# Kernel tuning notes

Hardware: AMD Instinct MI355X
Metric: run time of the kernel (lower is better)

## Reference

```python
import jax, jax.numpy as jnp
import numpy as np

B, L, C = 2, 8192, 256
K, NLEV = 17, 4
HALF = K // 2


def setup_inputs() -> dict:
    key = jax.random.key(0)
    ks = jax.random.split(key, 10)
    s = 0.02
    return {
        "x": jax.random.normal(ks[0], (B, L, C), jnp.float32),
        "stem_w": jax.random.normal(ks[1], (C, C, 2), jnp.float32) * s,   # Conv1d (out,in,k)
        "stem_b": jax.random.normal(ks[2], (C,), jnp.float32) * s,
        "qkv_w": jax.random.normal(ks[3], (3 * C, C), jnp.float32) * s,
        "width_w": jax.random.normal(ks[4], (1, C), jnp.float32) * s,
        "width_b": jax.random.normal(ks[5], (1,), jnp.float32) * s,
        "out_w": jax.random.normal(ks[6], (C, C), jnp.float32) * s,
        "query": jax.random.normal(ks[7], (NLEV * C,), jnp.float32) * s,
        "film_w": jax.random.normal(ks[8], (2 * C, NLEV * C), jnp.float32) * s,
        "film_b": jax.random.normal(ks[9], (2 * C,), jnp.float32) * s,
    }


def _local_attn(h, qkv_w, width_w, width_b, out_w):
    # h: (b, l, c); 1D local windowed attention with learned sigmoid distance mask
    b, l, c = h.shape
    rel_dist = jnp.abs(jnp.arange(K, dtype=h.dtype) - HALF)  # (K,)
    max_dist = float(HALF)
    scale = c ** -0.5
    qkv = h @ qkv_w.T
    q, k, v = jnp.split(qkv, 3, axis=-1)
    width = jax.nn.sigmoid(h @ width_w.T + width_b) * max_dist + 0.5  # (b,l,1)
    k_pad = jnp.pad(k, ((0, 0), (HALF, HALF), (0, 0)))
    v_pad = jnp.pad(v, ((0, 0), (HALF, HALF), (0, 0)))
    idx = jnp.arange(l)[:, None] + jnp.arange(K)[None, :]  # (l,K) indices into padded seq
    k_win = k_pad[:, idx]  # (b,l,K,c)
    v_win = v_pad[:, idx]  # (b,l,K,c)
    scores = jnp.einsum('blc,blwc->blw', q, k_win) * scale
    soft_mask = jax.nn.sigmoid((width - rel_dist) * 5.0)  # (b,l,K)
    scores = scores - (1.0 - soft_mask) * 10000.0
    attn = jax.nn.softmax(scores, axis=-1)
    o = jnp.einsum('blw,blwc->blc', attn, v_win)
    return (o + v) @ out_w.T


def _forward(x, stem_w, stem_b, qkv_w, width_w, width_b, out_w, query, film_w, film_b):
    b, l, c = x.shape
    # stem conv: Conv1d(C, C, kernel=2, padding=1), then narrow to first l positions
    h = jnp.transpose(x, (0, 2, 1))  # (B,C,L)
    h = jax.lax.conv_general_dilated(h, stem_w, (1,), [(1, 1)],
                                     dimension_numbers=('NCH', 'OIH', 'NCH'))
    h = h[:, :, :l] + stem_b[None, :, None]
    h = jnp.transpose(h, (0, 2, 1))  # (B,L,C)
    levels = []
    for i in range(NLEV):
        h = _local_attn(h, qkv_w, width_w, width_b, out_w)
        levels.append(h)
        if i < NLEV - 1:  # avg_pool(kernel=2, stride=2)
            bl = h.shape[1]
            h = h.reshape(b, bl // 2, 2, c).mean(axis=2)
    # nearest upsample each coarser level back to L (factors are exact powers of 2)
    ups = [levels[0]]
    for lvl in levels[1:]:
        ups.append(jnp.repeat(lvl, l // lvl.shape[1], axis=1))
    concat = jnp.concatenate(ups, axis=-1)  # (B,L,NLEV*C)
    gattn = jax.nn.softmax(concat @ query, axis=-1)  # (B,L)
    global_ctx = jnp.einsum('bl,bld->bd', gattn, concat)  # (B,NLEV*C)
    film = global_ctx @ film_w.T + film_b  # (B,2C)
    scale_f, bias_f = jnp.split(film, 2, axis=-1)
    return levels[0] * (1.0 + scale_f[:, None, :]) + bias_f[:, None, :]


def reference(x, stem_w, stem_b, qkv_w, width_w, width_b, out_w, query, film_w, film_b):
    return _forward(x, stem_w, stem_b, qkv_w, width_w, width_b, out_w, query, film_w, film_b)
```

## Files before the change

kernel.cpp:

```cpp
#include <hip/hip_runtime.h>
#include <math.h>

#define L_SEQ 8192
#define B_SZ  2
#define CH    256
#define NLEV  4

typedef __attribute__((ext_vector_type(8))) short bf16x8;
typedef __attribute__((ext_vector_type(4))) float f32x4;

static __device__ __forceinline__ float sigmoidf_(float x) {
    return 1.0f / (1.0f + expf(-x));
}

static __device__ __forceinline__ float bf2f_(unsigned short u) {
    union { unsigned int ui; float f; } x;
    x.ui = ((unsigned int)u) << 16;
    return x.f;
}
static __device__ __forceinline__ unsigned short f2b_(float f) {
    union { float f; unsigned int u; } x;
    x.f = f;
    unsigned int lsb = (x.u >> 16) & 1u;
    unsigned int r = x.u + 0x7fffu + lsb;
    return (unsigned short)(r >> 16);
}
static __device__ __forceinline__ float4 ldb4_(const unsigned short* p) {
    ushort4 u = *(const ushort4*)p;
    return make_float4(bf2f_(u.x), bf2f_(u.y), bf2f_(u.z), bf2f_(u.w));
}

#define NPREP_BLOCKS 17409
__global__ __launch_bounds__(256) void prep_kernel(
    const float* __restrict__ x, const float* __restrict__ qkv_w,
    const float* __restrict__ out_w, const float* __restrict__ stem_w,
    unsigned short* __restrict__ x16g, unsigned short* __restrict__ qw16,
    unsigned short* __restrict__ sw16)
{
    __shared__ float owr[256];
    if (blockIdx.x >= NPREP_BLOCKS) {
        const int c = blockIdx.x - NPREP_BLOCKS, j = threadIdx.x;
        owr[j] = out_w[(size_t)c * 256 + j];
        __syncthreads();
        float acc = 0.0f;
        #pragma unroll 8
        for (int k = 0; k < 256; ++k)
            acc += owr[k] * qkv_w[(size_t)(512 + k) * 256 + j];
        qw16[(size_t)(512 + c) * 256 + j] = f2b_(acc);
        return;
    }
    int i = blockIdx.x * 256 + threadIdx.x;
    if (i < 256) { x16g[i] = 0; return; }
    i -= 256;
    if (i < 4194304) { x16g[256 + i] = f2b_(x[i]); return; }
    i -= 4194304;
    if (i < 131072) { qw16[i] = f2b_(qkv_w[i]); return; }
    i -= 131072;
    {
        int k = i & 511, nn = i >> 9;
        float v = (k < 256) ? stem_w[(size_t)nn * 512 + k * 2]
                            : stem_w[(size_t)nn * 512 + (k - 256) * 2 + 1];
        sw16[i] = f2b_(v);
    }
}

template<int STEM>
__global__ __launch_bounds__(512, 2) void level_fused_kernel(
    const unsigned short* __restrict__ h16in, const unsigned short* __restrict__ x16g,
    const unsigned short* __restrict__ sw, const float* __restrict__ sbias,
    const unsigned short* __restrict__ qw,
    const float* __restrict__ ww, const float* __restrict__ wbp,
    unsigned short* __restrict__ l16o, unsigned short* __restrict__ dsB, int l)
{
    __shared__ __align__(16) char smem[127232];
    unsigned short* hs = (unsigned short*)smem;
    unsigned short* xs = (unsigned short*)(smem + 40960);
    unsigned short* qs = (unsigned short*)(smem + 40960);
    unsigned short* ks = (unsigned short*)(smem + 73728);
    unsigned short* vt = (unsigned short*)(smem + 40960);
    unsigned short* pb = (unsigned short*)(smem + 114688);
    float* sp1 = (float*)(smem + 118784);
    float* ws1 = (float*)(smem + 126976);

    const int tid  = threadIdx.x;
    const int wave = tid >> 6;
    const int lane = tid & 63;
    const int rt   = wave & 3;
    const int half = wave >> 2;
    const int q    = lane >> 4;
    const int n    = lane & 15;

    int bid = blockIdx.x;
    const int cpx = gridDim.x >> 3;
    bid = (bid & 7) * cpx + (bid >> 3);

    const int bps = l >> 6;
    const int b  = bid / bps;
    const int t0 = (bid % bps) << 6;
    const size_t seqbase = (size_t)b * l;
    const int row0 = t0 + rt * 16;
    const int ct0 = wave * 2;

    if constexpr (STEM) {
        #pragma unroll
        for (int i = 0; i < 6; ++i) {
            const int task = i * 512 + tid;
            if (task < 2592) {
                const int r = task >> 5, ch = task & 31;
                const int gx = t0 - 9 + r;
                const unsigned short* src = (gx >= 0 && gx < l)
                    ? x16g + ((size_t)(seqbase + gx) + 1) * 256 + ((ch ^ (r & 7)) << 3)
                    : x16g;
                __builtin_amdgcn_global_load_lds(
                    (const __attribute__((address_space(1))) void*)src,
                    (__attribute__((address_space(3))) void*)
                        (xs + (size_t)(i * 512 + (tid & ~63)) * 8),
                    16, 0, 0);
            }
        }
        __syncthreads();

        f32x4 accA[5] = {}, accB[5] = {};
        #pragma unroll
        for (int pass = 0; pass < 2; ++pass) {
            bf16x8 wA[8], wB[8];
            const unsigned short* wa_ = sw + (size_t)(ct0 * 16 + n) * 512 + pass * 256 + q * 8;
            const unsigned short* wb_ = sw + (size_t)((ct0 + 1) * 16 + n) * 512 + pass * 256 + q * 8;
            #pragma unroll
            for (int j = 0; j < 8; ++j) {
                wA[j] = *(const bf16x8*)(wa_ + j * 32);
                wB[j] = *(const bf16x8*)(wb_ + j * 32);
            }
            #pragma unroll
            for (int rtile = 0; rtile < 5; ++rtile) {
                const int xr = rtile * 16 + n + pass;
                const int xswz = (xr & 7) << 4;
                bf16x8 af[8];
                #pragma unroll
                for (int j = 0; j < 8; ++j)
                    af[j] = *(const bf16x8*)((const char*)xs +
                             ((xr * 512 + (j * 32 + q * 8) * 2) ^ xswz));
                #pragma unroll
                for (int j = 0; j < 8; ++j) {
                    accA[rtile] = __builtin_amdgcn_mfma_f32_16x16x32_bf16(af[j], wA[j], accA[rtile], 0, 0, 0);
                    accB[rtile] = __builtin_amdgcn_mfma_f32_16x16x32_bf16(af[j], wB[j], accB[rtile], 0, 0, 0);
                }
            }
        }
        const float bA = sbias[ct0 * 16 + n];
        const float bB = sbias[(ct0 + 1) * 16 + n];
        #pragma unroll
        for (int rtile = 0; rtile < 5; ++rtile)
            #pragma unroll
            for (int idx = 0; idx < 4; ++idx) {
                const int row = rtile * 16 + q * 4 + idx;
                const int growh = t0 - 8 + row;
                const int rswz = (row & 7) << 4;
                const bool ok = (growh >= 0 && growh < l);
                *(unsigned short*)((char*)hs +
                    ((row * 512 + (ct0 * 16 + n) * 2) ^ rswz)) =
                        ok ? f2b_(accA[rtile][idx] + bA) : (unsigned short)0;
                *(unsigned short*)((char*)hs +
                    ((row * 512 + ((ct0 + 1) * 16 + n) * 2) ^ rswz)) =
                        ok ? f2b_(accB[rtile][idx] + bB) : (unsigned short)0;
            }
        __syncthreads();
    } else {
        #pragma unroll
        for (int i = 0; i < 5; ++i) {
            const int task = i * 512 + tid;
            const int r = task >> 5, ch = task & 31;
            const int grow = t0 - 8 + r;
            const unsigned short* src = (grow >= 0 && grow < l)
                ? h16in + (seqbase + grow) * 256 + ((ch ^ (r & 7)) << 3)
                : x16g;
            __builtin_amdgcn_global_load_lds(
                (const __attribute__((address_space(1))) void*)src,
                (__attribute__((address_space(3))) void*)
                    (hs + (size_t)(i * 512 + (tid & ~63)) * 8),
                16, 0, 0);
        }
        __syncthreads();
    }

    {
        bf16x8 bwa[8], bwb[8];
        const unsigned short* wa_ = qw + (size_t)(ct0 * 16 + n) * 256 + q * 8;
        const unsigned short* wb_ = qw + (size_t)((ct0 + 1) * 16 + n) * 256 + q * 8;
        #pragma unroll
        for (int j = 0; j < 8; ++j) {
            bwa[j] = *(const bf16x8*)(wa_ + j * 32);
            bwb[j] = *(const bf16x8*)(wb_ + j * 32);
        }
        #pragma unroll
        for (int rtq = 0; rtq < 4; ++rtq) {
            const int hr = 8 + rtq * 16 + n;
            const int hswz = (hr & 7) << 4;
            bf16x8 af[8];
            #pragma unroll
            for (int j = 0; j < 8; ++j)
                af[j] = *(const bf16x8*)((const char*)hs +
                         ((hr * 512 + (j * 32 + q * 8) * 2) ^ hswz));
            f32x4 aA = {}, aB = {};
            #pragma unroll
            for (int j = 0; j < 8; ++j) {
                aA = __builtin_amdgcn_mfma_f32_16x16x32_bf16(af[j], bwa[j], aA, 0, 0, 0);
                aB = __builtin_amdgcn_mfma_f32_16x16x32_bf16(af[j], bwb[j], aB, 0, 0, 0);
            }
            #pragma unroll
            for (int idx = 0; idx < 4; ++idx) {
                const int row = rtq * 16 + q * 4 + idx;
                const int rswz = (row & 7) << 4;
                *(unsigned short*)((char*)qs +
                    ((row * 512 + (ct0 * 16 + n) * 2) ^ rswz)) = f2b_(aA[idx]);
                *(unsigned short*)((char*)qs +
                    ((row * 512 + ((ct0 + 1) * 16 + n) * 2) ^ rswz)) = f2b_(aB[idx]);
            }
        }
    }
    {
        bf16x8 bwa[8], bwb[8];
        const unsigned short* wa_ = qw + (size_t)(256 + ct0 * 16 + n) * 256 + q * 8;
        const unsigned short* wb_ = qw + (size_t)(256 + (ct0 + 1) * 16 + n) * 256 + q * 8;
        #pragma unroll
        for (int j = 0; j < 8; ++j) {
            bwa[j] = *(const bf16x8*)(wa_ + j * 32);
            bwb[j] = *(const bf16x8*)(wb_ + j * 32);
        }
        #pragma unroll
        for (int rtk = 0; rtk < 5; ++rtk) {
            const int hr = rtk * 16 + n;
            const int hswz = (hr & 7) << 4;
            bf16x8 af[8];
            #pragma unroll
            for (int j = 0; j < 8; ++j)
                af[j] = *(const bf16x8*)((const char*)hs +
                         ((hr * 512 + (j * 32 + q * 8) * 2) ^ hswz));
            f32x4 aA = {}, aB = {};
            #pragma unroll
            for (int j = 0; j < 8; ++j) {
                aA = __builtin_amdgcn_mfma_f32_16x16x32_bf16(af[j], bwa[j], aA, 0, 0, 0);
                aB = __builtin_amdgcn_mfma_f32_16x16x32_bf16(af[j], bwb[j], aB, 0, 0, 0);
            }
            #pragma unroll
            for (int idx = 0; idx < 4; ++idx) {
                const int row = rtk * 16 + q * 4 + idx;
                const int rswz = (row & 7) << 4;
                *(unsigned short*)((char*)ks +
                    ((row * 512 + (ct0 * 16 + n) * 2) ^ rswz)) = f2b_(aA[idx]);
                *(unsigned short*)((char*)ks +
                    ((row * 512 + ((ct0 + 1) * 16 + n) * 2) ^ rswz)) = f2b_(aB[idx]);
            }
        }
    }
    __syncthreads();

    const int kc0 = half * 128;
    float wdot = 0.0f;
    {
        const int hr = 8 + rt * 16 + n;
        const int hswz = (hr & 7) << 4;
        #pragma unroll
        for (int jj = 0; jj < 4; ++jj) {
            bf16x8 hv = *(const bf16x8*)((const char*)hs +
                        ((hr * 512 + (kc0 + q * 32 + jj * 8) * 2) ^ hswz));
            float4 wa = *((const float4*)(ww + kc0 + q * 32 + jj * 8));
            float4 wc = *((const float4*)(ww + kc0 + q * 32 + jj * 8 + 4));
            wdot += bf2f_((unsigned short)hv[0]) * wa.x
                  + bf2f_((unsigned short)hv[1]) * wa.y
                  + bf2f_((unsigned short)hv[2]) * wa.z
                  + bf2f_((unsigned short)hv[3]) * wa.w
                  + bf2f_((unsigned short)hv[4]) * wc.x
                  + bf2f_((unsigned short)hv[5]) * wc.y
                  + bf2f_((unsigned short)hv[6]) * wc.z
                  + bf2f_((unsigned short)hv[7]) * wc.w;
        }
    }
    wdot += __shfl_xor(wdot, 16, 64);
    wdot += __shfl_xor(wdot, 32, 64);
    if (half == 1 && q == 0) ws1[rt * 16 + n] = wdot;

    f32x4 accS[2] = {};
    {
        const int qrow = rt * 16 + n;
        const int qswz = (qrow & 7) << 4;
        bf16x8 qf[4];
        #pragma unroll
        for (int j = 0; j < 4; ++j)
            qf[j] = *(const bf16x8*)((const char*)qs +
                     ((qrow * 512 + (kc0 + q * 8 + j * 32) * 2) ^ qswz));
        #pragma unroll
        for (int h = 0; h < 2; ++h) {
            const int rk = rt * 16 + h * 16 + n;
            const int kswz = (rk & 7) << 4;
            #pragma unroll
            for (int j = 0; j < 4; ++j) {
                bf16x8 kb = *(const bf16x8*)((const char*)ks +
                            ((rk * 512 + (kc0 + q * 8 + j * 32) * 2) ^ kswz));
                accS[h] = __builtin_amdgcn_mfma_f32_16x16x32_bf16(
                    qf[j], kb, accS[h], 0, 0, 0);
            }
        }
    }
    if (half == 1) {
        *(f32x4*)(sp1 + ((rt * 2 + 0) * 64 + lane) * 4) = accS[0];
        *(f32x4*)(sp1 + ((rt * 2 + 1) * 64 + lane) * 4) = accS[1];
    }
    __syncthreads();

    if (half == 0) {
        accS[0] += *(const f32x4*)(sp1 + ((rt * 2 + 0) * 64 + lane) * 4);
        accS[1] += *(const f32x4*)(sp1 + ((rt * 2 + 1) * 64 + lane) * 4);
        const float w_n = sigmoidf_(wdot + ws1[rt * 16 + n] + wbp[0]) * 8.0f + 0.5f;

        float wd[4];
        #pragma unroll
        for (int r = 0; r < 4; ++r) wd[r] = __shfl(w_n, q * 4 + r, 64);

        float s[2][4];
        #pragma unroll
        for (int h = 0; h < 2; ++h)
            #pragma unroll
            for (int r = 0; r < 4; ++r) {
                int ii = q * 4 + r;
                int c  = h * 16 + n;
                int w  = c - ii;
                float dist = fabsf((float)w - 8.0f);
                float sm = sigmoidf_((wd[r] - dist) * 5.0f);
                float v = accS[h][r] * 0.0625f - (1.0f - sm) * 10000.0f;
                s[h][r] = (w >= 0 && w <= 16) ? v : -3.0e38f;
            }

        float mx[4], sum[4];
        #pragma unroll
        for (int r = 0; r < 4; ++r) mx[r] = fmaxf(s[0][r], s[1][r]);
        #pragma unroll
        for (int m = 1; m < 16; m <<= 1)
            #pragma unroll
            for (int r = 0; r < 4; ++r) mx[r] = fmaxf(mx[r], __shfl_xor(mx[r], m, 64));
        float e[2][4];
        #pragma unroll
        for (int h = 0; h < 2; ++h)
            #pragma unroll
            for (int r = 0; r < 4; ++r) e[h][r] = expf(s[h][r] - mx[r]);
        #pragma unroll
        for (int r = 0; r < 4; ++r) sum[r] = e[0][r] + e[1][r];
        #pragma unroll
        for (int m = 1; m < 16; m <<= 1)
            #pragma unroll
            for (int r = 0; r < 4; ++r) sum[r] += __shfl_xor(sum[r], m, 64);

        #pragma unroll
        for (int h = 0; h < 2; ++h)
            #pragma unroll
            for (int r = 0; r < 4; ++r) {
                int ii = q * 4 + r, c = h * 16 + n;
                float p = e[h][r] / sum[r];
                if (c == ii + 8) p += 1.0f;
                pb[rt * 512 + ii * 32 + c] = f2b_(p);
            }
    }
    __syncthreads();

    {
        bf16x8 bwa[8], bwb[8];
        const unsigned short* wa_ = qw + (size_t)(512 + ct0 * 16 + n) * 256 + q * 8;
        const unsigned short* wb_ = qw + (size_t)(512 + (ct0 + 1) * 16 + n) * 256 + q * 8;
        #pragma unroll
        for (int j = 0; j < 8; ++j) {
            bwa[j] = *(const bf16x8*)(wa_ + j * 32);
            bwb[j] = *(const bf16x8*)(wb_ + j * 32);
        }
        #pragma unroll
        for (int rtv = 0; rtv < 5; ++rtv) {
            const int hr = rtv * 16 + n;
            const int hswz = (hr & 7) << 4;
            bf16x8 af[8];
            #pragma unroll
            for (int j = 0; j < 8; ++j)
                af[j] = *(const bf16x8*)((const char*)hs +
                         ((hr * 512 + (j * 32 + q * 8) * 2) ^ hswz));
            f32x4 aA = {}, aB = {};
            #pragma unroll
            for (int j = 0; j < 8; ++j) {
                aA = __builtin_amdgcn_mfma_f32_16x16x32_bf16(af[j], bwa[j], aA, 0, 0, 0);
                aB = __builtin_amdgcn_mfma_f32_16x16x32_bf16(af[j], bwb[j], aB, 0, 0, 0);
            }
            ushort4 pA, pB;
            pA.x = f2b_(aA[0]); pA.y = f2b_(aA[1]); pA.z = f2b_(aA[2]); pA.w = f2b_(aA[3]);
            pB.x = f2b_(aB[0]); pB.y = f2b_(aB[1]); pB.z = f2b_(aB[2]); pB.w = f2b_(aB[3]);
            const int rb = rtv * 16 + q * 4;
            *(ushort4*)(vt + (size_t)(ct0 * 16 + n) * 88 + rb) = pA;
            *(ushort4*)(vt + (size_t)((ct0 + 1) * 16 + n) * 88 + rb) = pB;
        }
    }
    __syncthreads();

    bf16x8 pf = *(const bf16x8*)(pb + rt * 512 + n * 32 + q * 8);
    const int rl = q * 4;
    const size_t gbase = seqbase + row0;
    #pragma unroll
    for (int c = 0; c < 8; ++c) {
        const int ct = half * 8 + c;
        bf16x8 vf = *(const bf16x8*)(vt + (ct * 16 + n) * 88 + rt * 16 + q * 8);
        f32x4 z = {};
        f32x4 o = __builtin_amdgcn_mfma_f32_16x16x32_bf16(pf, vf, z, 0, 0, 0);
        const int col = ct * 16 + n;
        float v0 = o[0], v1 = o[1], v2 = o[2], v3 = o[3];
        size_t r0 = (gbase + rl) * CH + col;
        l16o[r0]          = f2b_(v0);
        l16o[r0 + CH]     = f2b_(v1);
        l16o[r0 + 2 * CH] = f2b_(v2);
        l16o[r0 + 3 * CH] = f2b_(v3);
        if (dsB) {
            size_t d0 = ((gbase + rl) >> 1) * CH + col;
            dsB[d0]      = f2b_(0.5f * (v0 + v1));
            dsB[d0 + CH] = f2b_(0.5f * (v2 + v3));
        }
    }
}

__global__ __launch_bounds__(1024) void tail_ctx_kernel(
    const unsigned short* __restrict__ l0, const unsigned short* __restrict__ l1,
    const unsigned short* __restrict__ l2, const unsigned short* __restrict__ l3,
    const float* __restrict__ query, float* __restrict__ partials,
    float* __restrict__ denomP)
{
    __shared__ float eS[128];
    const int tid = threadIdx.x;
    const int chunk = blockIdx.x, b = blockIdx.y;
    const int t0 = chunk * 128;
    const unsigned short* levp[4] = {l0, l1, l2, l3};

    const int w = tid >> 6, lane = tid & 63;
    const int lev = lane >> 4, c0 = (lane & 15) * 16;
    const unsigned short* lpbase = levp[lev] + (size_t)b * (L_SEQ >> lev) * CH;
    const float* qp = query + lev * CH + c0;
    float4 q0 = *(const float4*)(qp);
    float4 q1 = *(const float4*)(qp + 4);
    float4 q2 = *(const float4*)(qp + 8);
    float4 q3 = *(const float4*)(qp + 12);
    #pragma unroll
    for (int j = 0; j < 8; ++j) {
        int t = t0 + w * 8 + j;
        const unsigned short* p = lpbase + (size_t)(t >> lev) * CH + c0;
        float4 h0 = ldb4_(p), h1 = ldb4_(p + 4), h2 = ldb4_(p + 8), h3 = ldb4_(p + 12);
        float part = h0.x * q0.x + h0.y * q0.y + h0.z * q0.z + h0.w * q0.w
                   + h1.x * q1.x + h1.y * q1.y + h1.z * q1.z + h1.w * q1.w
                   + h2.x * q2.x + h2.y * q2.y + h2.z * q2.z + h2.w * q2.w
                   + h3.x * q3.x + h3.y * q3.y + h3.z * q3.z + h3.w * q3.w;
        #pragma unroll
        for (int m = 1; m < 64; m <<= 1) part += __shfl_xor(part, m, 64);
        if (lane == 0) eS[w * 8 + j] = expf(part);
    }
    __syncthreads();

    if (tid == 0) {
        float ds = 0.0f;
        #pragma unroll 8
        for (int i = 0; i < 128; ++i) ds += eS[i];
        denomP[b * 64 + chunk] = ds;
    }

    const int dlev = tid >> 8, c = tid & 255;
    const unsigned short* lp = levp[dlev] + (size_t)b * (L_SEQ >> dlev) * CH;
    float acc = 0.0f;
    #pragma unroll 4
    for (int t = t0; t < t0 + 128; ++t)
        acc += eS[t - t0] * bf2f_(lp[(size_t)(t >> dlev) * CH + c]);
    partials[(size_t)(b * 64 + chunk) * 1024 + tid] = acc;
}

__global__ __launch_bounds__(256) void film_kernel(
    const float* __restrict__ partials, const float* __restrict__ denomP,
    const float* __restrict__ fw, const float* __restrict__ fb,
    float* __restrict__ film)
{
    __shared__ float ctxS[2048];
    const int tid = threadIdx.x;

    float den[2];
    #pragma unroll
    for (int b = 0; b < 2; ++b) {
        float d = 0.0f;
        #pragma unroll
        for (int c = 0; c < 64; ++c) d += denomP[b * 64 + c];
        den[b] = d;
    }
    #pragma unroll
    for (int v = 0; v < 8; ++v) {
        const int idx = v * 256 + tid;
        const int b = idx >> 10, d = idx & 1023;
        float acc = 0.0f;
        #pragma unroll
        for (int c = 0; c < 64; ++c)
            acc += partials[(size_t)(b * 64 + c) * 1024 + d];
        ctxS[idx] = acc / den[b];
    }
    __syncthreads();

    const int lane = tid & 63;
    const int j = blockIdx.x * 4 + (tid >> 6);
    float acc0 = 0.0f, acc1 = 0.0f;
    #pragma unroll
    for (int r = 0; r < 4; ++r) {
        float4 w4 = *((const float4*)(fw + (size_t)j * 1024 + r * 256) + lane);
        float4 c0 = *((const float4*)(ctxS + r * 256) + lane);
        float4 c1 = *((const float4*)(ctxS + 1024 + r * 256) + lane);
        acc0 += w4.x * c0.x + w4.y * c0.y + w4.z * c0.z + w4.w * c0.w;
        acc1 += w4.x * c1.x + w4.y * c1.y + w4.z * c1.z + w4.w * c1.w;
    }
    #pragma unroll
    for (int m = 1; m < 64; m <<= 1) {
        acc0 += __shfl_xor(acc0, m, 64);
        acc1 += __shfl_xor(acc1, m, 64);
    }
    if (lane == 0) {
        float b = fb[j];
        film[j] = acc0 + b;
        film[512 + j] = acc1 + b;
    }
}

__global__ void final_kernel(const unsigned short* __restrict__ lev0,
                             const float* __restrict__ film,
                             float* __restrict__ out)
{
    size_t n4 = ((size_t)blockIdx.x * 256 + threadIdx.x) * 4;
    int c = (int)(n4 & (CH - 1));
    int b = (int)(n4 >> 21);
    float4 h = ldb4_(lev0 + n4);
    const float* fs = film + b * 512;
    float4 o;
    o.x = h.x * (1.0f + fs[c + 0]) + fs[256 + c + 0];
    o.y = h.y * (1.0f + fs[c + 1]) + fs[256 + c + 1];
    o.z = h.z * (1.0f + fs[c + 2]) + fs[256 + c + 2];
    o.w = h.w * (1.0f + fs[c + 3]) + fs[256 + c + 3];
    *(float4*)(out + n4) = o;
}

extern "C" void kernel_launch(void* const* d_in, const int* in_sizes, int n_in,
                              void* d_out, int out_size, void* d_ws, size_t ws_size,
                              hipStream_t stream) {
    const float* x       = (const float*)d_in[0];
    const float* stem_w  = (const float*)d_in[1];
    const float* stem_b  = (const float*)d_in[2];
    const float* qkv_w   = (const float*)d_in[3];
    const float* width_w = (const float*)d_in[4];
    const float* width_b = (const float*)d_in[5];
    const float* out_w   = (const float*)d_in[6];
    const float* query   = (const float*)d_in[7];
    const float* film_w  = (const float*)d_in[8];
    const float* film_b  = (const float*)d_in[9];
    float* out = (float*)d_out;
    float* ws  = (float*)d_ws;

    float* partials = ws;
    float* denomP   = partials + 131072;
    float* ctx      = denomP + 128;
    float* film     = ctx + 2048;
    unsigned short* x16g  = (unsigned short*)(film + 1024);
    unsigned short* h16_0 = x16g + 4194560;
    unsigned short* h16_1 = h16_0 + 4194304;
    unsigned short* h16_2 = h16_1 + 2097152;
    unsigned short* h16_3 = h16_2 + 1048576;
    unsigned short* qkv16 = h16_3 + 524288;
    unsigned short* ov16  = qkv16 + 12582912;
    unsigned short* l16_0 = ov16 + 4194304;
    unsigned short* l16_1 = l16_0 + 4194304;
    unsigned short* l16_2 = l16_1 + 2097152;
    unsigned short* l16_3 = l16_2 + 1048576;
    unsigned short* qw16  = l16_3 + 524288;
    unsigned short* ow16  = qw16 + 196608;
    unsigned short* sw16  = ow16 + 65536;
    unsigned short* h16[4]  = {h16_0, h16_1, h16_2, h16_3};
    unsigned short* l16[4]  = {l16_0, l16_1, l16_2, l16_3};
    (void)qkv16; (void)ov16; (void)ow16; (void)ctx;

    prep_kernel<<<NPREP_BLOCKS + 256, 256, 0, stream>>>(
        x, qkv_w, out_w, stem_w, x16g, qw16, sw16);

    for (int i = 0; i < NLEV; ++i) {
        const int l = L_SEQ >> i;
        const int M = B_SZ * l;
        if (i == 0)
            level_fused_kernel<1><<<M / 64, 512, 0, stream>>>(
                h16[0], x16g, sw16, stem_b, qw16, width_w, width_b,
                l16[0], h16_1, l);
        else
            level_fused_kernel<0><<<M / 64, 512, 0, stream>>>(
                h16[i], x16g, sw16, stem_b, qw16, width_w, width_b,
                l16[i], (i < NLEV - 1) ? h16[i + 1] : nullptr, l);
    }

    tail_ctx_kernel<<<dim3(64, B_SZ), 1024, 0, stream>>>(
        l16_0, l16_1, l16_2, l16_3, query, partials, denomP);
    film_kernel<<<128, 256, 0, stream>>>(partials, denomP, film_w, film_b, film);
    final_kernel<<<(B_SZ * L_SEQ * CH) / 1024, 256, 0, stream>>>(l16_0, film, out);
}
```

Before: 225.5 us.

## Double block to 1024 threads with one column tile per wave

The fused level kernel now launches 1024 threads (16 waves) per block instead of 512. Each wave handles one 16-column output tile in the stem, Q, K and V projections instead of two, and the PV output stage is split across all 16 waves. Only 8 waves do the score and width work and 4 do the softmax, so some waves sit idle during those phases. The aim is more waves per block to hide latency and halve per-wave register use. Shared memory of about 127 KB per block already limited residency, so one larger block replaces the two smaller ones per CU.

```diff
diff --git a/kernel.cpp b/kernel.cpp
--- a/kernel.cpp
+++ b/kernel.cpp
@@ -65,7 +65,7 @@
 }
 
 template<int STEM>
-__global__ __launch_bounds__(512, 2) void level_fused_kernel(
+__global__ __launch_bounds__(1024, 1) void level_fused_kernel(
     const unsigned short* __restrict__ h16in, const unsigned short* __restrict__ x16g,
     const unsigned short* __restrict__ sw, const float* __restrict__ sbias,
     const unsigned short* __restrict__ qw,
@@ -85,10 +85,11 @@
     const int tid  = threadIdx.x;
     const int wave = tid >> 6;
     const int lane = tid & 63;
-    const int rt   = wave & 3;
-    const int half = wave >> 2;
+    const int rt8  = wave & 3;
+    const int half = (wave >> 2) & 1;
     const int q    = lane >> 4;
     const int n    = lane & 15;
+    const int ct   = wave;
 
     int bid = blockIdx.x;
     const int cpx = gridDim.x >> 3;
@@ -98,13 +99,11 @@
     const int b  = bid / bps;
     const int t0 = (bid % bps) << 6;
     const size_t seqbase = (size_t)b * l;
-    const int row0 = t0 + rt * 16;
-    const int ct0 = wave * 2;
 
     if constexpr (STEM) {
         #pragma unroll
-        for (int i = 0; i < 6; ++i) {
-            const int task = i * 512 + tid;
+        for (int i = 0; i < 3; ++i) {
+            const int task = i * 1024 + tid;
             if (task < 2592) {
                 const int r = task >> 5, ch = task & 31;
                 const int gx = t0 - 9 + r;
@@ -114,23 +113,19 @@
                 __builtin_amdgcn_global_load_lds(
                     (const __attribute__((address_space(1))) void*)src,
                     (__attribute__((address_space(3))) void*)
-                        (xs + (size_t)(i * 512 + (tid & ~63)) * 8),
+                        (xs + (size_t)(i * 1024 + (tid & ~63)) * 8),
                     16, 0, 0);
             }
         }
         __syncthreads();
 
-        f32x4 accA[5] = {}, accB[5] = {};
+        f32x4 accA[5] = {};
         #pragma unroll
         for (int pass = 0; pass < 2; ++pass) {
-            bf16x8 wA[8], wB[8];
-            const unsigned short* wa_ = sw + (size_t)(ct0 * 16 + n) * 512 + pass * 256 + q * 8;
-            const unsigned short* wb_ = sw + (size_t)((ct0 + 1) * 16 + n) * 512 + pass * 256 + q * 8;
-            #pragma unroll
-            for (int j = 0; j < 8; ++j) {
-                wA[j] = *(const bf16x8*)(wa_ + j * 32);
-                wB[j] = *(const bf16x8*)(wb_ + j * 32);
-            }
+            bf16x8 wA[8];
+            const unsigned short* wa_ = sw + (size_t)(ct * 16 + n) * 512 + pass * 256 + q * 8;
+            #pragma unroll
+            for (int j = 0; j < 8; ++j) wA[j] = *(const bf16x8*)(wa_ + j * 32);
             #pragma unroll
             for (int rtile = 0; rtile < 5; ++rtile) {
                 const int xr = rtile * 16 + n + pass;
@@ -141,14 +136,12 @@
                     af[j] = *(const bf16x8*)((const char*)xs +
                              ((xr * 512 + (j * 32 + q * 8) * 2) ^ xswz));
                 #pragma unroll
-                for (int j = 0; j < 8; ++j) {
-                    accA[rtile] = __builtin_amdgcn_mfma_f32_16x16x32_bf16(af[j], wA[j], accA[rtile], 0, 0, 0);
-                    accB[rtile] = __builtin_amdgcn_mfma_f32_16x16x32_bf16(af[j], wB[j], accB[rtile], 0, 0, 0);
-                }
-            }
-        }
-        const float bA = sbias[ct0 * 16 + n];
-        const float bB = sbias[(ct0 + 1) * 16 + n];
+                for (int j = 0; j < 8; ++j)
+                    accA[rtile] = __builtin_amdgcn_mfma_f32_16x16x32_bf16(
+                        af[j], wA[j], accA[rtile], 0, 0, 0);
+            }
+        }
+        const float bA = sbias[ct * 16 + n];
         #pragma unroll
         for (int rtile = 0; rtile < 5; ++rtile)
             #pragma unroll
@@ -158,40 +151,35 @@
                 const int rswz = (row & 7) << 4;
                 const bool ok = (growh >= 0 && growh < l);
                 *(unsigned short*)((char*)hs +
-                    ((row * 512 + (ct0 * 16 + n) * 2) ^ rswz)) =
+                    ((row * 512 + (ct * 16 + n) * 2) ^ rswz)) =
                         ok ? f2b_(accA[rtile][idx] + bA) : (unsigned short)0;
-                *(unsigned short*)((char*)hs +
-                    ((row * 512 + ((ct0 + 1) * 16 + n) * 2) ^ rswz)) =
-                        ok ? f2b_(accB[rtile][idx] + bB) : (unsigned short)0;
             }
         __syncthreads();
     } else {
         #pragma unroll
-        for (int i = 0; i < 5; ++i) {
-            const int task = i * 512 + tid;
-            const int r = task >> 5, ch = task & 31;
-            const int grow = t0 - 8 + r;
-            const unsigned short* src = (grow >= 0 && grow < l)
-                ? h16in + (seqbase + grow) * 256 + ((ch ^ (r & 7)) << 3)
-                : x16g;
-            __builtin_amdgcn_global_load_lds(
-                (const __attribute__((address_space(1))) void*)src,
-                (__attribute__((address_space(3))) void*)
-                    (hs + (size_t)(i * 512 + (tid & ~63)) * 8),
-                16, 0, 0);
+        for (int i = 0; i < 3; ++i) {
+            const int task = i * 1024 + tid;
+            if (task < 2560) {
+                const int r = task >> 5, ch = task & 31;
+                const int grow = t0 - 8 + r;
+                const unsigned short* src = (grow >= 0 && grow < l)
+                    ? h16in + (seqbase + grow) * 256 + ((ch ^ (r & 7)) << 3)
+                    : x16g;
+                __builtin_amdgcn_global_load_lds(
+                    (const __attribute__((address_space(1))) void*)src,
+                    (__attribute__((address_space(3))) void*)
+                        (hs + (size_t)(i * 1024 + (tid & ~63)) * 8),
+                    16, 0, 0);
+            }
         }
         __syncthreads();
     }
 
     {
-        bf16x8 bwa[8], bwb[8];
-        const unsigned short* wa_ = qw + (size_t)(ct0 * 16 + n) * 256 + q * 8;
-        const unsigned short* wb_ = qw + (size_t)((ct0 + 1) * 16 + n) * 256 + q * 8;
-        #pragma unroll
-        for (int j = 0; j < 8; ++j) {
-            bwa[j] = *(const bf16x8*)(wa_ + j * 32);
-            bwb[j] = *(const bf16x8*)(wb_ + j * 32);
-        }
+        bf16x8 bwa[8];
+        const unsigned short* wa_ = qw + (size_t)(ct * 16 + n) * 256 + q * 8;
+        #pragma unroll
+        for (int j = 0; j < 8; ++j) bwa[j] = *(const bf16x8*)(wa_ + j * 32);
         #pragma unroll
         for (int rtq = 0; rtq < 4; ++rtq) {
             const int hr = 8 + rtq * 16 + n;
@@ -201,32 +189,24 @@
             for (int j = 0; j < 8; ++j)
                 af[j] = *(const bf16x8*)((const char*)hs +
                          ((hr * 512 + (j * 32 + q * 8) * 2) ^ hswz));
-            f32x4 aA = {}, aB = {};
-            #pragma unroll
-            for (int j = 0; j < 8; ++j) {
+            f32x4 aA = {};
+            #pragma unroll
+            for (int j = 0; j < 8; ++j)
                 aA = __builtin_amdgcn_mfma_f32_16x16x32_bf16(af[j], bwa[j], aA, 0, 0, 0);
-                aB = __builtin_amdgcn_mfma_f32_16x16x32_bf16(af[j], bwb[j], aB, 0, 0, 0);
-            }
             #pragma unroll
             for (int idx = 0; idx < 4; ++idx) {
                 const int row = rtq * 16 + q * 4 + idx;
                 const int rswz = (row & 7) << 4;
                 *(unsigned short*)((char*)qs +
-                    ((row * 512 + (ct0 * 16 + n) * 2) ^ rswz)) = f2b_(aA[idx]);
-                *(unsigned short*)((char*)qs +
-                    ((row * 512 + ((ct0 + 1) * 16 + n) * 2) ^ rswz)) = f2b_(aB[idx]);
+                    ((row * 512 + (ct * 16 + n) * 2) ^ rswz)) = f2b_(aA[idx]);
             }
         }
     }
     {
-        bf16x8 bwa[8], bwb[8];
-        const unsigned short* wa_ = qw + (size_t)(256 + ct0 * 16 + n) * 256 + q * 8;
-        const unsigned short* wb_ = qw + (size_t)(256 + (ct0 + 1) * 16 + n) * 256 + q * 8;
-        #pragma unroll
-        for (int j = 0; j < 8; ++j) {
-            bwa[j] = *(const bf16x8*)(wa_ + j * 32);
-            bwb[j] = *(const bf16x8*)(wb_ + j * 32);
-        }
+        bf16x8 bwa[8];
+        const unsigned short* wa_ = qw + (size_t)(256 + ct * 16 + n) * 256 + q * 8;
+        #pragma unroll
+        for (int j = 0; j < 8; ++j) bwa[j] = *(const bf16x8*)(wa_ + j * 32);
         #pragma unroll
         for (int rtk = 0; rtk < 5; ++rtk) {
             const int hr = rtk * 16 + n;
@@ -236,82 +216,80 @@
             for (int j = 0; j < 8; ++j)
                 af[j] = *(const bf16x8*)((const char*)hs +
                          ((hr * 512 + (j * 32 + q * 8) * 2) ^ hswz));
-            f32x4 aA = {}, aB = {};
-            #pragma unroll
-            for (int j = 0; j < 8; ++j) {
+            f32x4 aA = {};
+            #pragma unroll
+            for (int j = 0; j < 8; ++j)
                 aA = __builtin_amdgcn_mfma_f32_16x16x32_bf16(af[j], bwa[j], aA, 0, 0, 0);
-                aB = __builtin_amdgcn_mfma_f32_16x16x32_bf16(af[j], bwb[j], aB, 0, 0, 0);
-            }
             #pragma unroll
             for (int idx = 0; idx < 4; ++idx) {
                 const int row = rtk * 16 + q * 4 + idx;
                 const int rswz = (row & 7) << 4;
                 *(unsigned short*)((char*)ks +
-                    ((row * 512 + (ct0 * 16 + n) * 2) ^ rswz)) = f2b_(aA[idx]);
-                *(unsigned short*)((char*)ks +
-                    ((row * 512 + ((ct0 + 1) * 16 + n) * 2) ^ rswz)) = f2b_(aB[idx]);
+                    ((row * 512 + (ct * 16 + n) * 2) ^ rswz)) = f2b_(aA[idx]);
             }
         }
     }
     __syncthreads();
 
-    const int kc0 = half * 128;
     float wdot = 0.0f;
-    {
-        const int hr = 8 + rt * 16 + n;
-        const int hswz = (hr & 7) << 4;
-        #pragma unroll
-        for (int jj = 0; jj < 4; ++jj) {
-            bf16x8 hv = *(const bf16x8*)((const char*)hs +
-                        ((hr * 512 + (kc0 + q * 32 + jj * 8) * 2) ^ hswz));
-            float4 wa = *((const float4*)(ww + kc0 + q * 32 + jj * 8));
-            float4 wc = *((const float4*)(ww + kc0 + q * 32 + jj * 8 + 4));
-            wdot += bf2f_((unsigned short)hv[0]) * wa.x
-                  + bf2f_((unsigned short)hv[1]) * wa.y
-                  + bf2f_((unsigned short)hv[2]) * wa.z
-                  + bf2f_((unsigned short)hv[3]) * wa.w
-                  + bf2f_((unsigned short)hv[4]) * wc.x
-                  + bf2f_((unsigned short)hv[5]) * wc.y
-                  + bf2f_((unsigned short)hv[6]) * wc.z
-                  + bf2f_((unsigned short)hv[7]) * wc.w;
-        }
-    }
-    wdot += __shfl_xor(wdot, 16, 64);
-    wdot += __shfl_xor(wdot, 32, 64);
-    if (half == 1 && q == 0) ws1[rt * 16 + n] = wdot;
-
     f32x4 accS[2] = {};
-    {
-        const int qrow = rt * 16 + n;
-        const int qswz = (qrow & 7) << 4;
-        bf16x8 qf[4];
-        #pragma unroll
-        for (int j = 0; j < 4; ++j)
-            qf[j] = *(const bf16x8*)((const char*)qs +
-                     ((qrow * 512 + (kc0 + q * 8 + j * 32) * 2) ^ qswz));
-        #pragma unroll
-        for (int h = 0; h < 2; ++h) {
-            const int rk = rt * 16 + h * 16 + n;
-            const int kswz = (rk & 7) << 4;
-            #pragma unroll
-            for (int j = 0; j < 4; ++j) {
-                bf16x8 kb = *(const bf16x8*)((const char*)ks +
-                            ((rk * 512 + (kc0 + q * 8 + j * 32) * 2) ^ kswz));
-                accS[h] = __builtin_amdgcn_mfma_f32_16x16x32_bf16(
-                    qf[j], kb, accS[h], 0, 0, 0);
-            }
-        }
-    }
-    if (half == 1) {
-        *(f32x4*)(sp1 + ((rt * 2 + 0) * 64 + lane) * 4) = accS[0];
-        *(f32x4*)(sp1 + ((rt * 2 + 1) * 64 + lane) * 4) = accS[1];
+    if (wave < 8) {
+        const int kc0 = half * 128;
+        {
+            const int hr = 8 + rt8 * 16 + n;
+            const int hswz = (hr & 7) << 4;
+            #pragma unroll
+            for (int jj = 0; jj < 4; ++jj) {
+                bf16x8 hv = *(const bf16x8*)((const char*)hs +
+                            ((hr * 512 + (kc0 + q * 32 + jj * 8) * 2) ^ hswz));
+                float4 wa = *((const float4*)(ww + kc0 + q * 32 + jj * 8));
+                float4 wc = *((const float4*)(ww + kc0 + q * 32 + jj * 8 + 4));
+                wdot += bf2f_((unsigned short)hv[0]) * wa.x
+                      + bf2f_((unsigned short)hv[1]) * wa.y
+                      + bf2f_((unsigned short)hv[2]) * wa.z
+                      + bf2f_((unsigned short)hv[3]) * wa.w
+                      + bf2f_((unsigned short)hv[4]) * wc.x
+                      + bf2f_((unsigned short)hv[5]) * wc.y
+                      + bf2f_((unsigned short)hv[6]) * wc.z
+                      + bf2f_((unsigned short)hv[7]) * wc.w;
+            }
+        }
+        wdot += __shfl_xor(wdot, 16, 64);
+        wdot += __shfl_xor(wdot, 32, 64);
+        if (half == 1 && q == 0) ws1[rt8 * 16 + n] = wdot;
+
+        {
+            const int qrow = rt8 * 16 + n;
+            const int qswz = (qrow & 7) << 4;
+            bf16x8 qf[4];
+            #pragma unroll
+            for (int j = 0; j < 4; ++j)
+                qf[j] = *(const bf16x8*)((const char*)qs +
+                         ((qrow * 512 + (kc0 + q * 8 + j * 32) * 2) ^ qswz));
+            #pragma unroll
+            for (int h = 0; h < 2; ++h) {
+                const int rk = rt8 * 16 + h * 16 + n;
+                const int kswz = (rk & 7) << 4;
+                #pragma unroll
+                for (int j = 0; j < 4; ++j) {
+                    bf16x8 kb = *(const bf16x8*)((const char*)ks +
+                                ((rk * 512 + (kc0 + q * 8 + j * 32) * 2) ^ kswz));
+                    accS[h] = __builtin_amdgcn_mfma_f32_16x16x32_bf16(
+                        qf[j], kb, accS[h], 0, 0, 0);
+                }
+            }
+        }
+        if (half == 1) {
+            *(f32x4*)(sp1 + ((rt8 * 2 + 0) * 64 + lane) * 4) = accS[0];
+            *(f32x4*)(sp1 + ((rt8 * 2 + 1) * 64 + lane) * 4) = accS[1];
+        }
     }
     __syncthreads();
 
-    if (half == 0) {
-        accS[0] += *(const f32x4*)(sp1 + ((rt * 2 + 0) * 64 + lane) * 4);
-        accS[1] += *(const f32x4*)(sp1 + ((rt * 2 + 1) * 64 + lane) * 4);
-        const float w_n = sigmoidf_(wdot + ws1[rt * 16 + n] + wbp[0]) * 8.0f + 0.5f;
+    if (wave < 4) {
+        accS[0] += *(const f32x4*)(sp1 + ((rt8 * 2 + 0) * 64 + lane) * 4);
+        accS[1] += *(const f32x4*)(sp1 + ((rt8 * 2 + 1) * 64 + lane) * 4);
+        const float w_n = sigmoidf_(wdot + ws1[rt8 * 16 + n] + wbp[0]) * 8.0f + 0.5f;
 
         float wd[4];
         #pragma unroll
@@ -357,20 +335,16 @@
                 int ii = q * 4 + r, c = h * 16 + n;
                 float p = e[h][r] / sum[r];
                 if (c == ii + 8) p += 1.0f;
-                pb[rt * 512 + ii * 32 + c] = f2b_(p);
+                pb[rt8 * 512 + ii * 32 + c] = f2b_(p);
             }
     }
     __syncthreads();
 
     {
-        bf16x8 bwa[8], bwb[8];
-        const unsigned short* wa_ = qw + (size_t)(512 + ct0 * 16 + n) * 256 + q * 8;
-        const unsigned short* wb_ = qw + (size_t)(512 + (ct0 + 1) * 16 + n) * 256 + q * 8;
-        #pragma unroll
-        for (int j = 0; j < 8; ++j) {
-            bwa[j] = *(const bf16x8*)(wa_ + j * 32);
-            bwb[j] = *(const bf16x8*)(wb_ + j * 32);
-        }
+        bf16x8 bwa[8];
+        const unsigned short* wa_ = qw + (size_t)(512 + ct * 16 + n) * 256 + q * 8;
+        #pragma unroll
+        for (int j = 0; j < 8; ++j) bwa[j] = *(const bf16x8*)(wa_ + j * 32);
         #pragma unroll
         for (int rtv = 0; rtv < 5; ++rtv) {
             const int hr = rtv * 16 + n;
@@ -380,42 +354,43 @@
             for (int j = 0; j < 8; ++j)
                 af[j] = *(const bf16x8*)((const char*)hs +
                          ((hr * 512 + (j * 32 + q * 8) * 2) ^ hswz));
-            f32x4 aA = {}, aB = {};
-            #pragma unroll
-            for (int j = 0; j < 8; ++j) {
+            f32x4 aA = {};
+            #pragma unroll
+            for (int j = 0; j < 8; ++j)
                 aA = __builtin_amdgcn_mfma_f32_16x16x32_bf16(af[j], bwa[j], aA, 0, 0, 0);
-                aB = __builtin_amdgcn_mfma_f32_16x16x32_bf16(af[j], bwb[j], aB, 0, 0, 0);
-            }
-            ushort4 pA, pB;
+            ushort4 pA;
             pA.x = f2b_(aA[0]); pA.y = f2b_(aA[1]); pA.z = f2b_(aA[2]); pA.w = f2b_(aA[3]);
-            pB.x = f2b_(aB[0]); pB.y = f2b_(aB[1]); pB.z = f2b_(aB[2]); pB.w = f2b_(aB[3]);
             const int rb = rtv * 16 + q * 4;
-            *(ushort4*)(vt + (size_t)(ct0 * 16 + n) * 88 + rb) = pA;
-            *(ushort4*)(vt + (size_t)((ct0 + 1) * 16 + n) * 88 + rb) = pB;
+            *(ushort4*)(vt + (size_t)(ct * 16 + n) * 88 + rb) = pA;
         }
     }
     __syncthreads();
 
-    bf16x8 pf = *(const bf16x8*)(pb + rt * 512 + n * 32 + q * 8);
-    const int rl = q * 4;
-    const size_t gbase = seqbase + row0;
-    #pragma unroll
-    for (int c = 0; c < 8; ++c) {
-        const int ct = half * 8 + c;
-        bf16x8 vf = *(const bf16x8*)(vt + (ct * 16 + n) * 88 + rt * 16 + q * 8);
-        f32x4 z = {};
-        f32x4 o = __builtin_amdgcn_mfma_f32_16x16x32_bf16(pf, vf, z, 0, 0, 0);
-        const int col = ct * 16 + n;
-        float v0 = o[0], v1 = o[1], v2 = o[2], v3 = o[3];
-        size_t r0 = (gbase + rl) * CH + col;
-        l16o[r0]          = f2b_(v0);
-        l16o[r0 + CH]     = f2b_(v1);
-        l16o[r0 + 2 * CH] = f2b_(v2);
-        l16o[r0 + 3 * CH] = f2b_(v3);
-        if (dsB) {
-            size_t d0 = ((gbase + rl) >> 1) * CH + col;
-            dsB[d0]      = f2b_(0.5f * (v0 + v1));
-            dsB[d0 + CH] = f2b_(0.5f * (v2 + v3));
+    {
+        const int rtp = wave & 3;
+        const int ctq = wave >> 2;
+        bf16x8 pf = *(const bf16x8*)(pb + rtp * 512 + n * 32 + q * 8);
+        const int rl = q * 4;
+        const int row0 = t0 + rtp * 16;
+        const size_t gbase = seqbase + row0;
+        #pragma unroll
+        for (int c = 0; c < 4; ++c) {
+            const int ctp = ctq * 4 + c;
+            bf16x8 vf = *(const bf16x8*)(vt + (ctp * 16 + n) * 88 + rtp * 16 + q * 8);
+            f32x4 z = {};
+            f32x4 o = __builtin_amdgcn_mfma_f32_16x16x32_bf16(pf, vf, z, 0, 0, 0);
+            const int col = ctp * 16 + n;
+            float v0 = o[0], v1 = o[1], v2 = o[2], v3 = o[3];
+            size_t r0 = (gbase + rl) * CH + col;
+            l16o[r0]          = f2b_(v0);
+            l16o[r0 + CH]     = f2b_(v1);
+            l16o[r0 + 2 * CH] = f2b_(v2);
+            l16o[r0 + 3 * CH] = f2b_(v3);
+            if (dsB) {
+                size_t d0 = ((gbase + rl) >> 1) * CH + col;
+                dsB[d0]      = f2b_(0.5f * (v0 + v1));
+                dsB[d0 + CH] = f2b_(0.5f * (v2 + v3));
+            }
         }
     }
 }
@@ -584,11 +559,11 @@
         const int l = L_SEQ >> i;
         const int M = B_SZ * l;
         if (i == 0)
-            level_fused_kernel<1><<<M / 64, 512, 0, stream>>>(
+            level_fused_kernel<1><<<M / 64, 1024, 0, stream>>>(
                 h16[0], x16g, sw16, stem_b, qw16, width_w, width_b,
                 l16[0], h16_1, l);
         else
-            level_fused_kernel<0><<<M / 64, 512, 0, stream>>>(
+            level_fused_kernel<0><<<M / 64, 1024, 0, stream>>>(
                 h16[i], x16g, sw16, stem_b, qw16, width_w, width_b,
                 l16[i], (i < NLEV - 1) ? h16[i + 1] : nullptr, l);
     }
```

Measured after the change: 218.7 us. 3.0% less time.
